# Performance work log

Measured on AMD Instinct MI355X. Metric: run time of the kernel, lower is better.

## Reference

```python
import jax, jax.numpy as jnp
import numpy as np

EMBED_DIM = 512

def setup_inputs() -> dict:
    key = jax.random.key(0)
    ks = jax.random.split(key, 8)
    B, N, M, C = 4, 4096, 4096, EMBED_DIM
    s = 1.0 / np.sqrt(C)
    return {
        "rgb_features": jax.random.normal(ks[0], (B, N, C), jnp.float32),
        "depth_features": jax.random.normal(ks[1], (B, M, C), jnp.float32),
        "Wq": jax.random.normal(ks[2], (C, C), jnp.float32) * s,
        "bq": jnp.zeros((C,), jnp.float32),
        "Wk": jax.random.normal(ks[3], (C, C), jnp.float32) * s,
        "bk": jnp.zeros((C,), jnp.float32),
        "Wv": jax.random.normal(ks[4], (C, C), jnp.float32) * s,
        "bv": jnp.zeros((C,), jnp.float32),
    }

def reference(rgb_features, depth_features, Wq, bq, Wk, bk, Wv, bv):
    C = rgb_features.shape[-1]
    scale = C ** (-0.5)
    Q = rgb_features @ Wq + bq          # [B, N, C]
    K = depth_features @ Wk + bk        # [B, M, C]
    V = depth_features @ Wv + bv        # [B, M, C]
    scores = jnp.einsum('bnc,bmc->bnm', Q, K) * scale
    attn = jax.nn.softmax(scores, axis=-1)
    return jnp.einsum('bnm,bmc->bnc', attn, V)
```

## Files before the change

### kernel.cpp

```cpp
#include <hip/hip_runtime.h>
#include <hip/hip_bf16.h>
#include <stdint.h>


typedef unsigned short u16;
typedef __attribute__((ext_vector_type(8))) short bf16x8;
typedef __attribute__((ext_vector_type(16))) float f32x16;
typedef __attribute__((ext_vector_type(4))) unsigned short u16x4;

#define GLD_LDS16(g, l)                                                        \
  __builtin_amdgcn_global_load_lds(                                            \
      (const __attribute__((address_space(1))) unsigned int*)(g),              \
      (__attribute__((address_space(3))) unsigned int*)(l), 16, 0, 0)

__device__ __forceinline__ u16 f2bf(float f) {
  unsigned x = __float_as_uint(f);
  return (u16)((x + 0x7fffu + ((x >> 16) & 1u)) >> 16);
}
__device__ __forceinline__ float bf2f(short s) {
  return __uint_as_float((unsigned)(unsigned short)s << 16);
}

template <int TM, int TN, int BIAS_MODE, int OUT_MODE, int MINW>
__global__ __launch_bounds__(256, MINW) void gemm32(
    const u16* __restrict__ A, const u16* __restrict__ Bm,
    const float* __restrict__ bias, void* __restrict__ Cv, int M, int N, int K,
    long long sAb, long long sBb, long long sCb, float scale) {
  constexpr int WROWS = TM / 2;
  constexpr int WCOLS = TN / 2;
  constexpr int MSUB = WROWS / 32;
  constexpr int NSUB = WCOLS / 32;
  constexpr int CA = TM / 64;
  constexpr int CB = TN / 64;

  const int bz = blockIdx.z;
  A += (size_t)bz * sAb;
  Bm += (size_t)bz * sBb;

  const int bm = blockIdx.y * TM;
  const int bn = blockIdx.x * TN;

  __shared__ u16 As[2][TM * 32];
  __shared__ u16 Bs[2][TN * 32];

  const int tid = threadIdx.x;
  const int wave = tid >> 6;
  const int lane = tid & 63;
  const int ln31 = lane & 31;
  const int half = lane >> 5;
  const int wr = wave >> 1;
  const int wc = wave & 1;

  const int rowA = lane >> 2;
  const int swz = ((lane & 3) ^ ((rowA + (rowA >> 2)) & 3)) * 8;
  const int gl = (ln31 + (ln31 >> 2)) & 3;

  f32x16 acc[MSUB][NSUB] = {};

  auto stage = [&](int buf, int k0) {
#pragma unroll
    for (int r = 0; r < CA; ++r) {
      const int ch = wave * CA + r;
      GLD_LDS16(A + (size_t)(bm + ch * 16 + rowA) * K + k0 + swz,
                As[buf] + ch * 16 * 32);
    }
#pragma unroll
    for (int r = 0; r < CB; ++r) {
      const int ch = wave * CB + r;
      GLD_LDS16(Bm + (size_t)(bn + ch * 16 + rowA) * K + k0 + swz,
                Bs[buf] + ch * 16 * 32);
    }
  };

  const int niter = K >> 5;
  stage(0, 0);
  for (int it = 0; it < niter; ++it) {
    __syncthreads();
    if (it + 1 < niter) stage((it + 1) & 1, (it + 1) * 32);
    const int buf = it & 1;
#pragma unroll
    for (int kc = 0; kc < 2; ++kc) {
      const int p = ((kc * 2 + half) ^ gl) * 8;
      bf16x8 af[MSUB], bfv[NSUB];
#pragma unroll
      for (int mt = 0; mt < MSUB; ++mt)
        af[mt] =
            *(const bf16x8*)&As[buf][(wr * WROWS + mt * 32 + ln31) * 32 + p];
#pragma unroll
      for (int nt = 0; nt < NSUB; ++nt)
        bfv[nt] =
            *(const bf16x8*)&Bs[buf][(wc * WCOLS + nt * 32 + ln31) * 32 + p];
#pragma unroll
      for (int mt = 0; mt < MSUB; ++mt)
#pragma unroll
        for (int nt = 0; nt < NSUB; ++nt)
          acc[mt][nt] = __builtin_amdgcn_mfma_f32_32x32x16_bf16(
              af[mt], bfv[nt], acc[mt][nt], 0, 0, 0);
    }
  }

  const int crow0 = bm + wr * WROWS + 4 * half;
  const int ccol0 = bn + wc * WCOLS + ln31;
#pragma unroll
  for (int mt = 0; mt < MSUB; ++mt) {
#pragma unroll
    for (int nt = 0; nt < NSUB; ++nt) {
      const int col = ccol0 + nt * 32;
#pragma unroll
      for (int r = 0; r < 16; ++r) {
        const int row = crow0 + mt * 32 + (r & 3) + 8 * (r >> 2);
        float v = acc[mt][nt][r];
        if constexpr (BIAS_MODE == 1) v += bias[col];
        if constexpr (BIAS_MODE == 2) v += bias[row];
        const size_t idx = (size_t)bz * (size_t)sCb + (size_t)row * N + col;
        if constexpr (OUT_MODE == 0)
          ((u16*)Cv)[idx] = f2bf(v);
        else if constexpr (OUT_MODE == 1)
          ((float*)Cv)[idx] = v;
        else
          ((u16*)Cv)[idx] = f2bf(__expf(v * scale));
      }
    }
  }
}

#define XA_STGA(buf, j, k0)                                                    \
  GLD_LDS16(Ag + (size_t)((j) * 32 + (wv & 3) * 8 + (wv >> 2) * 128 + rlane) * \
                    512 +                                                      \
                (k0) + swz8,                                                   \
            &As[buf][((j) * 32 + (wv & 3) * 8 + (wv >> 2) * 128) * 64])
#define XA_STGB(buf, j, k0)                                                    \
  GLD_LDS16(Bg + (size_t)((j) * 64 + wv * 8 + rlane) * 512 + (k0) + swz8,      \
            &Bs[buf][((j) * 64 + wv * 8) * 64])

#define XA_PHASE(F, NV, PFS)                                                   \
  {                                                                            \
    bf16x8 af[4];                                                              \
    {                                                                          \
      const int arow = (wm * 128 + (F) * 32 + ln31) * 64;                      \
      _Pragma("unroll") for (int k = 0; k < 4; ++k) af[k] =                    \
          *(const bf16x8*)&As[p][arow + (((2 * k + half) ^ s7) << 3)];         \
    }                                                                          \
    if ((F) == 0) {                                                            \
      _Pragma("unroll") for (int n = 0; n < 2; ++n) {                          \
        const int brow = (wn * 64 + n * 32 + ln31) * 64;                       \
        _Pragma("unroll") for (int k = 0; k < 4; ++k) bfr[n][k] =              \
            *(const bf16x8*)&Bs[p][brow + (((2 * k + half) ^ s7) << 3)];       \
      }                                                                        \
    }                                                                          \
    PFS;                                                                       \
    __builtin_amdgcn_s_barrier();                                              \
    asm volatile("s_waitcnt lgkmcnt(0)" ::: "memory");                         \
    __builtin_amdgcn_sched_barrier(0);                                         \
    __builtin_amdgcn_s_setprio(1);                                             \
    _Pragma("unroll") for (int k = 0; k < 4; ++k) {                            \
      acc[F][0] = __builtin_amdgcn_mfma_f32_32x32x16_bf16(af[k], bfr[0][k],    \
                                                          acc[F][0], 0, 0, 0); \
      acc[F][1] = __builtin_amdgcn_mfma_f32_32x32x16_bf16(af[k], bfr[1][k],    \
                                                          acc[F][1], 0, 0, 0); \
    }                                                                          \
    __builtin_amdgcn_s_setprio(0);                                             \
    asm volatile("s_waitcnt vmcnt(" NV ")" ::: "memory");                      \
    __builtin_amdgcn_s_barrier();                                              \
    asm volatile("" ::: "memory");                                             \
  }

__global__ __launch_bounds__(512, 2) void gemm256_exp(
    const u16* __restrict__ Qm, const u16* __restrict__ Km,
    u16* __restrict__ Sout, long long sAb, long long sSb, float scale) {
  const int bz = blockIdx.z;
  const int bm = blockIdx.y * 256;
  const int bn = blockIdx.x * 256;
  const u16* Ag = Qm + (size_t)bz * (size_t)sAb + (size_t)bm * 512;
  const u16* Bg = Km + (size_t)bz * (size_t)sAb + (size_t)bn * 512;

  __shared__ u16 As[2][256 * 64];
  __shared__ u16 Bs[2][256 * 64];

  const int tid = threadIdx.x;
  const int wv = tid >> 6;
  const int lane = tid & 63;
  const int ln31 = lane & 31;
  const int half = lane >> 5;
  const int wm = wv >> 2;
  const int wn = wv & 3;
  const int rlane = lane >> 3;
  const int swz8 = ((lane & 7) ^ rlane) << 3;
  const int s7 = ln31 & 7;

  f32x16 acc[4][2] = {};
  bf16x8 bfr[2][4];

#pragma unroll
  for (int j = 0; j < 4; ++j) XA_STGB(0, j, 0);
#pragma unroll
  for (int j = 0; j < 4; ++j) XA_STGA(0, j, 0);
  asm volatile("s_waitcnt vmcnt(3)" ::: "memory");
  __builtin_amdgcn_s_barrier();
  asm volatile("" ::: "memory");

  for (int t = 0; t < 7; ++t) {
    const int p = t & 1;
    const int q = p ^ 1;
    const int kn = (t + 1) << 6;
    XA_PHASE(0, "4", { XA_STGB(q, 0, kn); XA_STGB(q, 1, kn); });
    XA_PHASE(1, "5", { XA_STGB(q, 2, kn); XA_STGB(q, 3, kn); });
    XA_PHASE(2, "6", { XA_STGA(q, 0, kn); XA_STGA(q, 1, kn); });
    XA_PHASE(3, "3", { XA_STGA(q, 2, kn); XA_STGA(q, 3, kn); });
  }
  {
    const int p = 1;
    XA_PHASE(0, "2", {});
    XA_PHASE(1, "1", {});
    XA_PHASE(2, "0", {});
    XA_PHASE(3, "0", {});
  }

  const size_t ob = (size_t)bz * (size_t)sSb;
  const int c0 = bn + wn * 64 + ln31;
  const int r0 = bm + wm * 128 + 4 * half;
#pragma unroll
  for (int m = 0; m < 4; ++m) {
#pragma unroll
    for (int n = 0; n < 2; ++n) {
      const int col = c0 + n * 32;
#pragma unroll
      for (int r = 0; r < 16; ++r) {
        const int row = r0 + m * 32 + (r & 3) + 8 * (r >> 2);
        Sout[ob + (size_t)row * 4096 + col] = f2bf(__expf(acc[m][n][r] * scale));
      }
    }
  }
}

#define PV_BODY(IT, NV, DO_STAGE, DO_TAIL)                                     \
  {                                                                            \
    const int buf = (IT) & 3;                                                  \
    if (DO_STAGE) stage(((IT) + 3) & 3, ((IT) + 3) * 32);                      \
    bf16x8 af[2][2], bfv[2][2];                                                \
    _Pragma("unroll") for (int kc = 0; kc < 2; ++kc) {                         \
      const int p = ((kc * 2 + half) ^ gl) * 8;                                \
      _Pragma("unroll") for (int mt = 0; mt < 2; ++mt)                         \
        af[kc][mt] = *(const bf16x8*)&As[buf][(mt * 32 + ln31) * 32 + p];      \
      _Pragma("unroll") for (int nt = 0; nt < 2; ++nt)                         \
        bfv[kc][nt] =                                                          \
            *(const bf16x8*)&Bs[buf][(wave * 64 + nt * 32 + ln31) * 32 + p];   \
    }                                                                          \
    __builtin_amdgcn_s_barrier();                                              \
    asm volatile("s_waitcnt lgkmcnt(0)" ::: "memory");                         \
    __builtin_amdgcn_sched_barrier(0);                                         \
    __builtin_amdgcn_s_setprio(1);                                             \
    _Pragma("unroll") for (int kc = 0; kc < 2; ++kc) {                         \
      _Pragma("unroll") for (int mt = 0; mt < 2; ++mt) {                       \
        dacc[mt] = __builtin_amdgcn_mfma_f32_32x32x16_bf16(                    \
            af[kc][mt], onesv, dacc[mt], 0, 0, 0);                             \
        _Pragma("unroll") for (int nt = 0; nt < 2; ++nt)                       \
          acc[mt][nt] = __builtin_amdgcn_mfma_f32_32x32x16_bf16(               \
              af[kc][mt], bfv[kc][nt], acc[mt][nt], 0, 0, 0);                  \
      }                                                                        \
    }                                                                          \
    __builtin_amdgcn_s_setprio(0);                                             \
    if (DO_TAIL) {                                                             \
      asm volatile("s_waitcnt vmcnt(" NV ")" ::: "memory");                    \
      __builtin_amdgcn_s_barrier();                                            \
      asm volatile("" ::: "memory");                                           \
    }                                                                          \
  }

__global__ __launch_bounds__(256, 2) void pv_gemm(
    const u16* __restrict__ P, const u16* __restrict__ Vt,
    float* __restrict__ O) {
  const int bz = blockIdx.z;
  const u16* A = P + (size_t)bz * (4096ull * 4096ull);
  const u16* B = Vt + (size_t)bz * (512ull * 4096ull);
  float* Ob = O + (size_t)bz * (4096ull * 512ull);

  const int bm = blockIdx.y * 64;
  const int bn = blockIdx.x * 256;

  __shared__ u16 As[4][64 * 32];
  __shared__ u16 Bs[4][256 * 32];

  const int tid = threadIdx.x;
  const int wave = tid >> 6;
  const int lane = tid & 63;
  const int ln31 = lane & 31;
  const int half = lane >> 5;

  const int rowA = lane >> 2;
  const int swz = ((lane & 3) ^ ((rowA + (rowA >> 2)) & 3)) * 8;
  const int gl = (ln31 + (ln31 >> 2)) & 3;

  f32x16 acc[2][2] = {};
  f32x16 dacc[2] = {};
  bf16x8 onesv;
#pragma unroll
  for (int j = 0; j < 8; ++j) onesv[j] = (short)0x3F80;

  auto stage = [&](int buf, int k0) {
    GLD_LDS16(A + (size_t)(bm + wave * 16 + rowA) * 4096 + k0 + swz,
              As[buf] + wave * 16 * 32);
#pragma unroll
    for (int r = 0; r < 4; ++r) {
      const int ch = wave * 4 + r;
      GLD_LDS16(B + (size_t)(bn + ch * 16 + rowA) * 4096 + k0 + swz,
                Bs[buf] + ch * 16 * 32);
    }
  };

  stage(0, 0);
  stage(1, 32);
  stage(2, 64);
  asm volatile("s_waitcnt vmcnt(10)" ::: "memory");
  __builtin_amdgcn_s_barrier();
  asm volatile("" ::: "memory");

  for (int it = 0; it < 125; ++it) PV_BODY(it, "10", true, true);
  PV_BODY(125, "5", false, true);
  PV_BODY(126, "0", false, true);
  PV_BODY(127, "0", false, false);

  const int crow0 = 4 * half;
  const int ccol0 = bn + wave * 64 + ln31;
#pragma unroll
  for (int mt = 0; mt < 2; ++mt) {
#pragma unroll
    for (int r = 0; r < 16; ++r) {
      const int rl = crow0 + mt * 32 + (r & 3) + 8 * (r >> 2);
      const float rd = 1.0f / dacc[mt][r];
#pragma unroll
      for (int nt = 0; nt < 2; ++nt)
        Ob[(size_t)(bm + rl) * 512 + ccol0 + nt * 32] = acc[mt][nt][r] * rd;
    }
  }
}

__global__ __launch_bounds__(256) void cvt_pair(const float* __restrict__ x,
                                                const float* __restrict__ y,
                                                u16* __restrict__ ox,
                                                u16* __restrict__ oy, int n4) {
  const int i = blockIdx.x * 256 + threadIdx.x;
  if (i >= n4) return;
  const float4 a = ((const float4*)x)[i];
  const float4 b = ((const float4*)y)[i];
  u16x4 oa, ob;
  oa[0] = f2bf(a.x); oa[1] = f2bf(a.y); oa[2] = f2bf(a.z); oa[3] = f2bf(a.w);
  ob[0] = f2bf(b.x); ob[1] = f2bf(b.y); ob[2] = f2bf(b.z); ob[3] = f2bf(b.w);
  ((u16x4*)ox)[i] = oa;
  ((u16x4*)oy)[i] = ob;
}

__global__ __launch_bounds__(256) void wtrans_k(const float* __restrict__ W,
                                                u16* __restrict__ WT) {
  const int tr = blockIdx.y * 64;
  const int tc = blockIdx.x * 64;
  __shared__ float T[64][65];
  const int t = threadIdx.x;
  const int r0 = t >> 4;
  const int c0 = (t & 15) * 4;
#pragma unroll
  for (int rr = 0; rr < 4; ++rr) {
    const int row = rr * 16 + r0;
    const float4 w = *(const float4*)&W[(size_t)(tr + row) * 512 + tc + c0];
    T[row][c0 + 0] = w.x; T[row][c0 + 1] = w.y;
    T[row][c0 + 2] = w.z; T[row][c0 + 3] = w.w;
  }
  __syncthreads();
#pragma unroll
  for (int rr = 0; rr < 4; ++rr) {
    const int orow = rr * 16 + r0;
    u16x4 o;
#pragma unroll
    for (int j = 0; j < 4; ++j) o[j] = f2bf(T[c0 + j][orow]);
    *(u16x4*)&WT[(size_t)(tc + orow) * 512 + tr + c0] = o;
  }
}

extern "C" void kernel_launch(void* const* d_in, const int* in_sizes, int n_in,
                              void* d_out, int out_size, void* d_ws,
                              size_t ws_size, hipStream_t stream) {
  const float* rgb = (const float*)d_in[0];
  const float* dep = (const float*)d_in[1];
  const float* Wq = (const float*)d_in[2];
  const float* bq = (const float*)d_in[3];
  const float* Wk = (const float*)d_in[4];
  const float* bk = (const float*)d_in[5];
  const float* Wv = (const float*)d_in[6];
  const float* bv = (const float*)d_in[7];
  float* out = (float*)d_out;

  const int B = 4, N = 4096, M = 4096, C = 512;
  const size_t nBNC = (size_t)B * N * C;
  const float scale = 0.044194173824159216f;

  char* ws = (char*)d_ws;
  size_t off = 0;
  auto carve = [&](size_t bytes) -> void* {
    void* p = ws + off;
    off += (bytes + 255) & ~(size_t)255;
    return p;
  };
  u16* rgb_bf = (u16*)carve(nBNC * 2);
  u16* dep_bf = (u16*)carve(nBNC * 2);
  u16* WqT = (u16*)carve((size_t)C * C * 2);
  u16* WkT = (u16*)carve((size_t)C * C * 2);
  u16* WvT = (u16*)carve((size_t)C * C * 2);
  u16* Qb = (u16*)carve(nBNC * 2);
  u16* Kb = (u16*)carve(nBNC * 2);
  u16* Vt = (u16*)carve(nBNC * 2);
  u16* Sb = (u16*)carve((size_t)B * N * M * 2);

  const long long strQ = (long long)N * C;
  const long long strS = (long long)N * M;
  const long long strV = (long long)C * M;

  cvt_pair<<<8192, 256, 0, stream>>>(rgb, dep, rgb_bf, dep_bf, (int)(nBNC / 4));
  wtrans_k<<<dim3(8, 8), 256, 0, stream>>>(Wq, WqT);
  wtrans_k<<<dim3(8, 8), 256, 0, stream>>>(Wk, WkT);
  wtrans_k<<<dim3(8, 8), 256, 0, stream>>>(Wv, WvT);

  gemm32<128, 128, 1, 0, 4><<<dim3(4, 128, 1), 256, 0, stream>>>(
      rgb_bf, WqT, bq, Qb, 16384, 512, 512, 0, 0, 0, 1.f);
  gemm32<128, 128, 1, 0, 4><<<dim3(4, 128, 1), 256, 0, stream>>>(
      dep_bf, WkT, bk, Kb, 16384, 512, 512, 0, 0, 0, 1.f);
  gemm32<128, 128, 2, 0, 4><<<dim3(32, 4, 4), 256, 0, stream>>>(
      WvT, dep_bf, bv, Vt, 512, 4096, 512, 0, strQ, strV, 1.f);

  gemm256_exp<<<dim3(16, 16, 4), 512, 0, stream>>>(Qb, Kb, Sb, strQ, strS,
                                                   scale);

  pv_gemm<<<dim3(2, 64, 4), 256, 0, stream>>>(Sb, Vt, out);
}
```

Measured before the change: 387.3 us.

## Enlarge PV GEMM tile to 128x256 with 8 waves and BK=64 triple buffering

The PV GEMM block tile grows from 64x256 with 4 waves to 128x256 with 8 waves arranged 2x4. The K step doubles to 64 with a 3-stage LDS ring instead of 4 stages of 32, and the swizzle is redone for 64-element rows. This raises reuse of the V tile per block and halves the number of barrier iterations, at the cost of more LDS per block (144KB) and possibly lower occupancy. The three weight-transpose launches are also merged into one kernel using a z grid dimension.

After: 370.2 us. 4.4% less time.

```diff
diff --git a/kernel.cpp b/kernel.cpp
--- a/kernel.cpp
+++ b/kernel.cpp
@@ -235,28 +235,29 @@
 
 #define PV_BODY(IT, NV, DO_STAGE, DO_TAIL)                                     \
   {                                                                            \
-    const int buf = (IT) & 3;                                                  \
-    if (DO_STAGE) stage(((IT) + 3) & 3, ((IT) + 3) * 32);                      \
-    bf16x8 af[2][2], bfv[2][2];                                                \
-    _Pragma("unroll") for (int kc = 0; kc < 2; ++kc) {                         \
-      const int p = ((kc * 2 + half) ^ gl) * 8;                                \
+    const int buf = (IT) % 3;                                                  \
+    if (DO_STAGE) stage(((IT) + 2) % 3, ((IT) + 2) * 64);                      \
+    bf16x8 af[4][2], bfv[4][2];                                                \
+    _Pragma("unroll") for (int k = 0; k < 4; ++k) {                            \
+      const int p = ((2 * k + half) ^ s7) << 3;                                \
       _Pragma("unroll") for (int mt = 0; mt < 2; ++mt)                         \
-        af[kc][mt] = *(const bf16x8*)&As[buf][(mt * 32 + ln31) * 32 + p];      \
+        af[k][mt] =                                                            \
+            *(const bf16x8*)&As[buf][(wm * 64 + mt * 32 + ln31) * 64 + p];     \
       _Pragma("unroll") for (int nt = 0; nt < 2; ++nt)                         \
-        bfv[kc][nt] =                                                          \
-            *(const bf16x8*)&Bs[buf][(wave * 64 + nt * 32 + ln31) * 32 + p];   \
+        bfv[k][nt] =                                                           \
+            *(const bf16x8*)&Bs[buf][(wn * 64 + nt * 32 + ln31) * 64 + p];     \
     }                                                                          \
     __builtin_amdgcn_s_barrier();                                              \
     asm volatile("s_waitcnt lgkmcnt(0)" ::: "memory");                         \
     __builtin_amdgcn_sched_barrier(0);                                         \
     __builtin_amdgcn_s_setprio(1);                                             \
-    _Pragma("unroll") for (int kc = 0; kc < 2; ++kc) {                         \
+    _Pragma("unroll") for (int k = 0; k < 4; ++k) {                            \
       _Pragma("unroll") for (int mt = 0; mt < 2; ++mt) {                       \
         dacc[mt] = __builtin_amdgcn_mfma_f32_32x32x16_bf16(                    \
-            af[kc][mt], onesv, dacc[mt], 0, 0, 0);                             \
+            af[k][mt], onesv, dacc[mt], 0, 0, 0);                              \
         _Pragma("unroll") for (int nt = 0; nt < 2; ++nt)                       \
           acc[mt][nt] = __builtin_amdgcn_mfma_f32_32x32x16_bf16(               \
-              af[kc][mt], bfv[kc][nt], acc[mt][nt], 0, 0, 0);                  \
+              af[k][mt], bfv[k][nt], acc[mt][nt], 0, 0, 0);                    \
       }                                                                        \
     }                                                                          \
     __builtin_amdgcn_s_setprio(0);                                             \
@@ -267,7 +268,7 @@
     }                                                                          \
   }
 
-__global__ __launch_bounds__(256, 2) void pv_gemm(
+__global__ __launch_bounds__(512, 2) void pv_gemm(
     const u16* __restrict__ P, const u16* __restrict__ Vt,
     float* __restrict__ O) {
   const int bz = blockIdx.z;
@@ -275,21 +276,22 @@
   const u16* B = Vt + (size_t)bz * (512ull * 4096ull);
   float* Ob = O + (size_t)bz * (4096ull * 512ull);
 
-  const int bm = blockIdx.y * 64;
+  const int bm = blockIdx.y * 128;
   const int bn = blockIdx.x * 256;
 
-  __shared__ u16 As[4][64 * 32];
-  __shared__ u16 Bs[4][256 * 32];
+  __shared__ u16 As[3][128 * 64];
+  __shared__ u16 Bs[3][256 * 64];
 
   const int tid = threadIdx.x;
-  const int wave = tid >> 6;
+  const int wv = tid >> 6;
   const int lane = tid & 63;
   const int ln31 = lane & 31;
   const int half = lane >> 5;
-
-  const int rowA = lane >> 2;
-  const int swz = ((lane & 3) ^ ((rowA + (rowA >> 2)) & 3)) * 8;
-  const int gl = (ln31 + (ln31 >> 2)) & 3;
+  const int wm = wv >> 2;
+  const int wn = wv & 3;
+  const int rlane = lane >> 3;
+  const int swz8 = ((lane & 7) ^ rlane) << 3;
+  const int s7 = ln31 & 7;
 
   f32x16 acc[2][2] = {};
   f32x16 dacc[2] = {};
@@ -298,30 +300,32 @@
   for (int j = 0; j < 8; ++j) onesv[j] = (short)0x3F80;
 
   auto stage = [&](int buf, int k0) {
-    GLD_LDS16(A + (size_t)(bm + wave * 16 + rowA) * 4096 + k0 + swz,
-              As[buf] + wave * 16 * 32);
+#pragma unroll
+    for (int r = 0; r < 2; ++r) {
+      const int ch = wv * 2 + r;
+      GLD_LDS16(A + (size_t)(bm + ch * 8 + rlane) * 4096 + k0 + swz8,
+                As[buf] + ch * 8 * 64);
+    }
 #pragma unroll
     for (int r = 0; r < 4; ++r) {
-      const int ch = wave * 4 + r;
-      GLD_LDS16(B + (size_t)(bn + ch * 16 + rowA) * 4096 + k0 + swz,
-                Bs[buf] + ch * 16 * 32);
+      const int ch = wv * 4 + r;
+      GLD_LDS16(B + (size_t)(bn + ch * 8 + rlane) * 4096 + k0 + swz8,
+                Bs[buf] + ch * 8 * 64);
     }
   };
 
   stage(0, 0);
-  stage(1, 32);
-  stage(2, 64);
-  asm volatile("s_waitcnt vmcnt(10)" ::: "memory");
+  stage(1, 64);
+  asm volatile("s_waitcnt vmcnt(6)" ::: "memory");
   __builtin_amdgcn_s_barrier();
   asm volatile("" ::: "memory");
 
-  for (int it = 0; it < 125; ++it) PV_BODY(it, "10", true, true);
-  PV_BODY(125, "5", false, true);
-  PV_BODY(126, "0", false, true);
-  PV_BODY(127, "0", false, false);
-
-  const int crow0 = 4 * half;
-  const int ccol0 = bn + wave * 64 + ln31;
+  for (int it = 0; it < 62; ++it) PV_BODY(it, "6", true, true);
+  PV_BODY(62, "0", false, true);
+  PV_BODY(63, "0", false, false);
+
+  const int crow0 = bm + wm * 64 + 4 * half;
+  const int ccol0 = bn + wn * 64 + ln31;
 #pragma unroll
   for (int mt = 0; mt < 2; ++mt) {
 #pragma unroll
@@ -330,7 +334,7 @@
       const float rd = 1.0f / dacc[mt][r];
 #pragma unroll
       for (int nt = 0; nt < 2; ++nt)
-        Ob[(size_t)(bm + rl) * 512 + ccol0 + nt * 32] = acc[mt][nt][r] * rd;
+        Ob[(size_t)rl * 512 + ccol0 + nt * 32] = acc[mt][nt][r] * rd;
     }
   }
 }
@@ -350,8 +354,13 @@
   ((u16x4*)oy)[i] = ob;
 }
 
-__global__ __launch_bounds__(256) void wtrans_k(const float* __restrict__ W,
-                                                u16* __restrict__ WT) {
+__global__ __launch_bounds__(256) void wtrans_k3(
+    const float* __restrict__ Wq, const float* __restrict__ Wk,
+    const float* __restrict__ Wv, u16* __restrict__ WqT,
+    u16* __restrict__ WkT, u16* __restrict__ WvT) {
+  const int z = blockIdx.z;
+  const float* W = z == 0 ? Wq : (z == 1 ? Wk : Wv);
+  u16* WT = z == 0 ? WqT : (z == 1 ? WkT : WvT);
   const int tr = blockIdx.y * 64;
   const int tc = blockIdx.x * 64;
   __shared__ float T[64][65];
@@ -415,9 +424,7 @@
   const long long strV = (long long)C * M;
 
   cvt_pair<<<8192, 256, 0, stream>>>(rgb, dep, rgb_bf, dep_bf, (int)(nBNC / 4));
-  wtrans_k<<<dim3(8, 8), 256, 0, stream>>>(Wq, WqT);
-  wtrans_k<<<dim3(8, 8), 256, 0, stream>>>(Wk, WkT);
-  wtrans_k<<<dim3(8, 8), 256, 0, stream>>>(Wv, WvT);
+  wtrans_k3<<<dim3(8, 8, 3), 256, 0, stream>>>(Wq, Wk, Wv, WqT, WkT, WvT);
 
   gemm32<128, 128, 1, 0, 4><<<dim3(4, 128, 1), 256, 0, stream>>>(
       rgb_bf, WqT, bq, Qb, 16384, 512, 512, 0, 0, 0, 1.f);
@@ -429,5 +436,5 @@
   gemm256_exp<<<dim3(16, 16, 4), 512, 0, stream>>>(Qb, Kb, Sb, strQ, strS,
                                                    scale);
 
-  pv_gemm<<<dim3(2, 64, 4), 256, 0, stream>>>(Sb, Vt, out);
-}
+  pv_gemm<<<dim3(2, 32, 4), 512, 0, stream>>>(Sb, Vt, out);
+}
```
